# Kernel optimization log

Hardware: AMD Instinct MI355X
Metric: run time of the kernel (lower is better)

The kernel has to match this reference:

```python
import jax, jax.numpy as jnp
import numpy as np

B, C, H, W = 8, 256, 64, 64
CM = C // 4          # mask channels (theta/phi out) = 64
CI = C - CM          # img channels = 192
EPS = 1e-5


def setup_inputs() -> dict:
    key = jax.random.key(0)
    ks = jax.random.split(key, 12)
    return {
        "x": jax.random.normal(ks[0], (B, C, H, W), dtype=jnp.float32),
        "g_w": jax.random.normal(ks[1], (C, C), dtype=jnp.float32) * 0.05,
        "g_b": jax.random.normal(ks[2], (C,), dtype=jnp.float32) * 0.01,
        "theta_w": jax.random.normal(ks[3], (CM, CM), dtype=jnp.float32) * 0.1,
        "theta_b": jax.random.normal(ks[4], (CM,), dtype=jnp.float32) * 0.01,
        "phi_w": jax.random.normal(ks[5], (CM, CI), dtype=jnp.float32) * 0.06,
        "phi_b": jax.random.normal(ks[6], (CM,), dtype=jnp.float32) * 0.01,
        "W_w": jax.random.normal(ks[7], (C, C), dtype=jnp.float32) * 0.05,
        "W_b": jax.random.normal(ks[8], (C,), dtype=jnp.float32) * 0.01,
        "bn_gamma": jax.random.normal(ks[9], (C,), dtype=jnp.float32) * 0.1 + 1.0,
        "bn_beta": jax.random.normal(ks[10], (C,), dtype=jnp.float32) * 0.01,
        "bn_mean": jax.random.normal(ks[11], (C,), dtype=jnp.float32) * 0.1,
        "bn_var": jnp.ones((C,), dtype=jnp.float32),
    }


def _conv1x1(t, w, b):
    # [B,Cin,H,W] x [Cout,Cin] -> [B,Cout,H,W]
    return jnp.einsum('bchw,oc->bohw', t, w) + b[None, :, None, None]


def _maxpool2(t):
    b, c, h, w = t.shape
    return t.reshape(b, c, h // 2, 2, w // 2, 2).max(axis=(3, 5))


def reference(x, g_w, g_b, theta_w, theta_b, phi_w, phi_b, W_w, W_b,
              bn_gamma, bn_beta, bn_mean, bn_var):
    b, c, h, w = x.shape
    ci = c // 4
    mask_ch = x[:, :ci]          # [B, C/4, H, W]
    img_ch = x[:, ci:]           # [B, 3C/4, H, W]

    # g: conv1x1 then 2x2 maxpool -> [B, C, N'] -> [B, N', C]
    g_x = _maxpool2(_conv1x1(x, g_w, g_b)).reshape(b, c, -1).transpose(0, 2, 1)
    # theta: conv1x1 on mask -> [B, N, C/4]
    theta_x = _conv1x1(mask_ch, theta_w, theta_b).reshape(b, ci, -1).transpose(0, 2, 1)
    # phi: conv1x1 on img then pool -> [B, C/4, N']
    phi_x = _maxpool2(_conv1x1(img_ch, phi_w, phi_b)).reshape(b, ci, -1)

    f = jnp.einsum('bnc,bcm->bnm', theta_x, phi_x)     # [B, N, N']
    f_div_C = jax.nn.softmax(f, axis=-1)
    y = jnp.einsum('bnm,bmc->bnc', f_div_C, g_x)       # [B, N, C]
    y = y.transpose(0, 2, 1).reshape(b, c, h, w)

    W_y = _conv1x1(y, W_w, W_b)
    # BatchNorm (inference form with running stats)
    inv = jax.lax.rsqrt(bn_var + EPS)
    W_y = (W_y - bn_mean[None, :, None, None]) * (inv * bn_gamma)[None, :, None, None] \
          + bn_beta[None, :, None, None]
    return W_y + x
```

## Files before the change

### kernel.cpp

```cpp
#include <hip/hip_runtime.h>
#include <hip/hip_bf16.h>

typedef __hip_bfloat16 bf16;
typedef unsigned short ushort;
typedef unsigned int uint;
typedef __attribute__((ext_vector_type(8))) short short8;
typedef __attribute__((ext_vector_type(4))) float f32x4;

#define Bn 8
#define Cn 256
#define Nn 4096
#define Mn 1024
#define EPSf 1e-5f

__device__ __forceinline__ float b2f(const bf16 v){ return __bfloat162float(v); }
__device__ __forceinline__ ushort f2bu(float f){
  uint u = __float_as_uint(f);
  return (ushort)((u + 0x7FFFu + ((u >> 16) & 1u)) >> 16);
}

__global__ __launch_bounds__(256) void transpose_kernel(
    const float* __restrict__ x, bf16* __restrict__ xT)
{
  __shared__ float xs[64][65];
  const int t = threadIdx.x;
  const int p0 = blockIdx.x*64, c0 = blockIdx.y*64, b = blockIdx.z;
  #pragma unroll
  for (int i = 0; i < 16; ++i) {
    int idx = t + i*256; int cl = idx >> 6, pl = idx & 63;
    xs[cl][pl] = x[((long)(b*Cn) + c0 + cl)*Nn + p0 + pl];
  }
  __syncthreads();
  ushort* xTu = (ushort*)xT;
  #pragma unroll
  for (int i = 0; i < 8; ++i) {
    int idx = t + i*256; int pl = idx >> 5, cp = idx & 31;
    uint u = (uint)f2bu(xs[cp*2][pl]) | ((uint)f2bu(xs[cp*2+1][pl]) << 16);
    *(uint*)(xTu + ((long)(b*Nn) + p0 + pl)*Cn + c0 + cp*2) = u;
  }
}

__global__ __launch_bounds__(256) void wcomb_kernel(
    const float* __restrict__ tw, const float* __restrict__ tb,
    const float* __restrict__ pw, const float* __restrict__ pb,
    const float* __restrict__ gw, const float* __restrict__ gb,
    bf16* __restrict__ Wcomb, float* __restrict__ bcomb)
{
  const int r = blockIdx.x, c = threadIdx.x;
  float v;
  if (r < 64)        v = (c < 64)  ? tw[r*64 + c]            : 0.f;
  else if (r < 128)  v = (c >= 64) ? pw[(r-64)*192 + (c-64)] : 0.f;
  else               v = gw[(r-128)*256 + c];
  Wcomb[r*256 + c] = __float2bfloat16(v);
  if (c == 0)
    bcomb[r] = (r < 64) ? tb[r] : (r < 128) ? pb[r-64] : gb[r-128];
}

__global__ __launch_bounds__(256) void gemm384_kernel(
    const bf16* __restrict__ xT, const bf16* __restrict__ Wcomb,
    const float* __restrict__ bcomb, bf16* __restrict__ Q,
    bf16* __restrict__ K, bf16* __restrict__ Vt)
{
  __shared__ union {
    struct { ushort As[128*40]; ushort Bs[128*40]; } g;
    float Pb[2][128][33];
  } sm;
  const int t = threadIdx.x;
  const int px = blockIdx.x, o0 = blockIdx.y*128, b = blockIdx.z;
  const int p0 = px*128;
  const int lane = t & 63, w = t >> 6;
  const int ql = lane & 15, quad = lane >> 4;
  const int wm = (w & 1)*64, wn = (w >> 1)*64;
  const ushort* xTu = (const ushort*)xT;
  const ushort* Wu  = (const ushort*)Wcomb;

  f32x4 acc[4][4];
  #pragma unroll
  for (int i = 0; i < 4; ++i)
    #pragma unroll
    for (int j = 0; j < 4; ++j) acc[i][j] = (f32x4){0.f,0.f,0.f,0.f};

  for (int kc = 0; kc < 8; ++kc) {
    __syncthreads();
    #pragma unroll
    for (int i = 0; i < 2; ++i) {
      int idx = t + i*256; int r = idx >> 2, cq = idx & 3;
      *(uint4*)(sm.g.As + r*40 + cq*8) =
          *(const uint4*)(xTu + ((long)(b*Nn) + p0 + r)*Cn + kc*32 + cq*8);
      *(uint4*)(sm.g.Bs + r*40 + cq*8) =
          *(const uint4*)(Wu + (o0 + r)*Cn + kc*32 + cq*8);
    }
    __syncthreads();
    short8 aF[4], bF[4];
    #pragma unroll
    for (int mi = 0; mi < 4; ++mi)
      aF[mi] = *(const short8*)(sm.g.As + (wm + mi*16 + ql)*40 + quad*8);
    #pragma unroll
    for (int ni = 0; ni < 4; ++ni)
      bF[ni] = *(const short8*)(sm.g.Bs + (wn + ni*16 + ql)*40 + quad*8);
    #pragma unroll
    for (int mi = 0; mi < 4; ++mi)
      #pragma unroll
      for (int ni = 0; ni < 4; ++ni)
        acc[mi][ni] = __builtin_amdgcn_mfma_f32_16x16x32_bf16(aF[mi], bF[ni], acc[mi][ni], 0, 0, 0);
  }
  float bias[4];
  #pragma unroll
  for (int ni = 0; ni < 4; ++ni) bias[ni] = bcomb[o0 + wn + ni*16 + ql];

  if (o0 == 0 && wn == 0) {
    #pragma unroll
    for (int mi = 0; mi < 4; ++mi)
      #pragma unroll
      for (int ni = 0; ni < 4; ++ni)
        #pragma unroll
        for (int r = 0; r < 4; ++r) {
          int p = p0 + wm + mi*16 + quad*4 + r;
          Q[((long)(b*Nn) + p)*64 + ni*16 + ql] = __float2bfloat16(acc[mi][ni][r] + bias[ni]);
        }
  }
  __syncthreads();
  if (o0 != 0 || wn == 64) {
    int g = w & 1;
    #pragma unroll
    for (int mi = 0; mi < 4; ++mi)
      #pragma unroll
      for (int ni = 0; ni < 4; ++ni) {
        float a0 = acc[mi][ni][0] + bias[ni], a1 = acc[mi][ni][1] + bias[ni];
        float a2 = acc[mi][ni][2] + bias[ni], a3 = acc[mi][ni][3] + bias[ni];
        int o = wn + ni*16 + ql;
        int wp = mi*8 + quad*2;
        sm.Pb[g][o][wp]     = fmaxf(a0, a1);
        sm.Pb[g][o][wp + 1] = fmaxf(a2, a3);
      }
  }
  __syncthreads();
  if (o0 == 0) {
    int wp = t & 31, og = t >> 5;
    ushort kv[8];
    #pragma unroll
    for (int j = 0; j < 8; ++j) {
      int o = 64 + og*8 + j;
      kv[j] = f2bu(fmaxf(sm.Pb[0][o][wp], sm.Pb[1][o][wp]));
    }
    *(uint4*)((ushort*)K + ((long)(b*Mn) + px*32 + wp)*64 + og*8) = *(uint4*)kv;
  } else {
    int ol = t >> 1, wp0 = (t & 1)*16;
    ushort vv[16];
    #pragma unroll
    for (int j = 0; j < 16; ++j)
      vv[j] = f2bu(fmaxf(sm.Pb[0][ol][wp0 + j], sm.Pb[1][ol][wp0 + j]));
    ushort* dst = (ushort*)Vt + ((long)(b*Cn) + (o0 - 128) + ol)*Mn + px*32 + wp0;
    *(uint4*)dst       = *(uint4*)(vv);
    *(uint4*)(dst + 8) = *(uint4*)(vv + 8);
  }
}

__global__ __launch_bounds__(256) void attn_kernel(
    const bf16* __restrict__ Q, const bf16* __restrict__ K, const bf16* __restrict__ Vt,
    bf16* __restrict__ Y)
{
  __shared__ __align__(16) ushort Ks[64*68];
  __shared__ __align__(16) ushort Vs[256*68];
  __shared__ __align__(16) ushort Ps[64*68];
  __shared__ float l_sh[64];

  const int t = threadIdx.x;
  const int b = blockIdx.y, q0 = blockIdx.x*64;
  const int lane = t & 63, w = t >> 6;
  const int ql = lane & 15, quad = lane >> 4;
  const int rql = w*16;
  const int pvr = (w & 1)*32;
  const int pvc = (w >> 1)*128;
  const ushort* Qu = (const ushort*)Q;
  const ushort* Ku = (const ushort*)K;
  const ushort* Vu = (const ushort*)Vt;

  const long qrow = (long)(b*Nn) + q0 + rql + ql;
  short8 aQ0 = *(const short8*)(Qu + qrow*64 + quad*8);
  short8 aQ1 = *(const short8*)(Qu + qrow*64 + 32 + quad*8);

  float lrow[4];
  #pragma unroll
  for (int r = 0; r < 4; ++r) lrow[r] = 0.f;

  f32x4 acc[2][8];
  #pragma unroll
  for (int mi = 0; mi < 2; ++mi)
    #pragma unroll
    for (int ci = 0; ci < 8; ++ci) acc[mi][ci] = (f32x4){0.f,0.f,0.f,0.f};

  for (int mt = 0; mt < 16; ++mt) {
    const int m0 = mt*64;
    __syncthreads();
    {
      int ch = t & 7, rr = t >> 3;
      #pragma unroll
      for (int i = 0; i < 2; ++i) {
        int row = rr + 32*i;
        *(uint4*)(Ks + row*68 + ch*8) =
            *(const uint4*)(Ku + ((long)(b*Mn) + m0 + row)*64 + ch*8);
      }
      #pragma unroll
      for (int p = 0; p < 8; ++p) {
        int n = rr + 32*p;
        *(uint4*)(Vs + n*68 + ch*8) =
            *(const uint4*)(Vu + ((long)(b*Cn) + n)*Mn + m0 + ch*8);
      }
    }
    __syncthreads();
    #pragma unroll
    for (int ct = 0; ct < 4; ++ct) {
      short8 b0 = *(const short8*)(Ks + (ct*16 + ql)*68 + quad*8);
      short8 b1 = *(const short8*)(Ks + (ct*16 + ql)*68 + 32 + quad*8);
      f32x4 s = (f32x4){0.f,0.f,0.f,0.f};
      s = __builtin_amdgcn_mfma_f32_16x16x32_bf16(aQ0, b0, s, 0, 0, 0);
      s = __builtin_amdgcn_mfma_f32_16x16x32_bf16(aQ1, b1, s, 0, 0, 0);
      #pragma unroll
      for (int r = 0; r < 4; ++r) {
        float e = __expf(s[r]);
        lrow[r] += e;
        Ps[(rql + quad*4 + r)*68 + ct*16 + ql] = f2bu(e);
      }
    }
    __syncthreads();
    short8 aP0[2], aP1[2];
    #pragma unroll
    for (int mi = 0; mi < 2; ++mi) {
      aP0[mi] = *(const short8*)(Ps + (pvr + mi*16 + ql)*68 + quad*8);
      aP1[mi] = *(const short8*)(Ps + (pvr + mi*16 + ql)*68 + 32 + quad*8);
    }
    #pragma unroll
    for (int ci = 0; ci < 8; ++ci) {
      short8 b0 = *(const short8*)(Vs + (pvc + ci*16 + ql)*68 + quad*8);
      short8 b1 = *(const short8*)(Vs + (pvc + ci*16 + ql)*68 + 32 + quad*8);
      #pragma unroll
      for (int mi = 0; mi < 2; ++mi) {
        acc[mi][ci] = __builtin_amdgcn_mfma_f32_16x16x32_bf16(aP0[mi], b0, acc[mi][ci], 0, 0, 0);
        acc[mi][ci] = __builtin_amdgcn_mfma_f32_16x16x32_bf16(aP1[mi], b1, acc[mi][ci], 0, 0, 0);
      }
    }
  }
  #pragma unroll
  for (int r = 0; r < 4; ++r)
    #pragma unroll
    for (int off = 1; off < 16; off <<= 1)
      lrow[r] += __shfl_xor(lrow[r], off, 64);
  if (ql == 0) {
    #pragma unroll
    for (int r = 0; r < 4; ++r) l_sh[rql + quad*4 + r] = lrow[r];
  }
  __syncthreads();
  #pragma unroll
  for (int mi = 0; mi < 2; ++mi)
    #pragma unroll
    for (int r = 0; r < 4; ++r) {
      int row = pvr + mi*16 + quad*4 + r;
      float inv = 1.f / l_sh[row];
      #pragma unroll
      for (int ci = 0; ci < 8; ++ci)
        Y[((long)(b*Nn) + q0 + row)*256 + pvc + ci*16 + ql] = __float2bfloat16(acc[mi][ci][r]*inv);
    }
}

__global__ __launch_bounds__(256) void wconv_kernel(
    const bf16* __restrict__ Y, const float* __restrict__ Ww, const float* __restrict__ Wb,
    const float* __restrict__ gamma, const float* __restrict__ beta,
    const float* __restrict__ mean, const float* __restrict__ var,
    const float* __restrict__ x, float* __restrict__ out)
{
  __shared__ __align__(16) ushort As[128*40];
  __shared__ __align__(16) ushort Bs[128*40];
  __shared__ float ssc[128], ssh[128];
  const int t = threadIdx.x;
  const int n0 = blockIdx.x*128, o0 = blockIdx.y*128, b = blockIdx.z;
  const int lane = t & 63, w = t >> 6;
  const int ql = lane & 15, quad = lane >> 4;
  const int wm = (w & 1)*64, wn = (w >> 1)*64;
  const ushort* Yu = (const ushort*)Y;

  if (t < 128) {
    int o = o0 + t;
    float sc = gamma[o] * rsqrtf(var[o] + EPSf);
    ssc[t] = sc;
    ssh[t] = (Wb[o] - mean[o])*sc + beta[o];
  }

  f32x4 acc[4][4];
  #pragma unroll
  for (int i = 0; i < 4; ++i)
    #pragma unroll
    for (int j = 0; j < 4; ++j) acc[i][j] = (f32x4){0.f,0.f,0.f,0.f};

  for (int kc = 0; kc < 8; ++kc) {
    __syncthreads();
    #pragma unroll
    for (int i = 0; i < 4; ++i) {
      int idx = t + i*256; int r = idx >> 3, cq = idx & 7;
      float4 v = *(const float4*)(Ww + (o0 + r)*Cn + kc*32 + cq*4);
      uint lo = (uint)f2bu(v.x) | ((uint)f2bu(v.y) << 16);
      uint hi = (uint)f2bu(v.z) | ((uint)f2bu(v.w) << 16);
      *(uint2*)(As + r*40 + cq*4) = make_uint2(lo, hi);
    }
    #pragma unroll
    for (int i = 0; i < 2; ++i) {
      int idx = t + i*256; int r = idx >> 2, cq = idx & 3;
      *(uint4*)(Bs + r*40 + cq*8) =
          *(const uint4*)(Yu + ((long)(b*Nn) + n0 + r)*Cn + kc*32 + cq*8);
    }
    __syncthreads();
    short8 aF[4], bF[4];
    #pragma unroll
    for (int mi = 0; mi < 4; ++mi)
      aF[mi] = *(const short8*)(As + (wm + mi*16 + ql)*40 + quad*8);
    #pragma unroll
    for (int ni = 0; ni < 4; ++ni)
      bF[ni] = *(const short8*)(Bs + (wn + ni*16 + ql)*40 + quad*8);
    #pragma unroll
    for (int mi = 0; mi < 4; ++mi)
      #pragma unroll
      for (int ni = 0; ni < 4; ++ni)
        acc[mi][ni] = __builtin_amdgcn_mfma_f32_16x16x32_bf16(aF[mi], bF[ni], acc[mi][ni], 0, 0, 0);
  }
  #pragma unroll
  for (int mi = 0; mi < 4; ++mi)
    #pragma unroll
    for (int r = 0; r < 4; ++r) {
      int ol = wm + mi*16 + quad*4 + r;
      int o = o0 + ol;
      float sc = ssc[ol], sh = ssh[ol];
      #pragma unroll
      for (int ni = 0; ni < 4; ++ni) {
        int n = n0 + wn + ni*16 + ql;
        long gidx = ((long)(b*Cn + o))*Nn + n;
        out[gidx] = acc[mi][ni][r]*sc + sh + x[gidx];
      }
    }
}

extern "C" void kernel_launch(void* const* d_in, const int* in_sizes, int n_in,
                              void* d_out, int out_size, void* d_ws, size_t ws_size,
                              hipStream_t stream)
{
  const float* x       = (const float*)d_in[0];
  const float* g_w     = (const float*)d_in[1];
  const float* g_b     = (const float*)d_in[2];
  const float* theta_w = (const float*)d_in[3];
  const float* theta_b = (const float*)d_in[4];
  const float* phi_w   = (const float*)d_in[5];
  const float* phi_b   = (const float*)d_in[6];
  const float* W_w     = (const float*)d_in[7];
  const float* W_b     = (const float*)d_in[8];
  const float* bn_g    = (const float*)d_in[9];
  const float* bn_b    = (const float*)d_in[10];
  const float* bn_m    = (const float*)d_in[11];
  const float* bn_v    = (const float*)d_in[12];
  float* out = (float*)d_out;

  bf16* wsb = (bf16*)d_ws;
  bf16* xT    = wsb;
  bf16* Y     = wsb;
  bf16* Q     = wsb + 8388608;
  bf16* K     = wsb + 10485760;
  bf16* Vt    = wsb + 11010048;
  bf16* Wcomb = wsb + 13107200;
  float* bcomb = (float*)(wsb + 13205504);

  transpose_kernel<<<dim3(64, 4, Bn), 256, 0, stream>>>(x, xT);
  wcomb_kernel<<<dim3(384), 256, 0, stream>>>(theta_w, theta_b, phi_w, phi_b, g_w, g_b, Wcomb, bcomb);
  gemm384_kernel<<<dim3(32, 3, Bn), 256, 0, stream>>>(xT, Wcomb, bcomb, Q, K, Vt);
  attn_kernel<<<dim3(64, Bn), 256, 0, stream>>>(Q, K, Vt, Y);
  wconv_kernel<<<dim3(32, 2, Bn), 256, 0, stream>>>(Y, W_w, W_b, bn_g, bn_b, bn_m, bn_v, x, out);
}
```

Baseline: 186.2 us.

## Use 512 threads per attention block, splitting score keys and PV columns across 8 waves

The attention kernel goes from 4 to 8 wavefronts per block. Each wave computes scores for half of the 64 keys in a tile and accumulates a 32x64 slice of the PV output instead of 32x128. Row sums are combined from two partial buffers in shared memory. This halves per-thread accumulator registers and cooperative load work, raising parallelism and latency hiding for the 512-block grid, at the cost of more threads contending at each barrier.

New measurement: 185.1 us. Within noise of the previous version (-0.6%).

```diff
diff --git a/kernel.cpp b/kernel.cpp
--- a/kernel.cpp
+++ b/kernel.cpp
@@ -156,27 +156,28 @@
   }
 }
 
-__global__ __launch_bounds__(256) void attn_kernel(
+__global__ __launch_bounds__(512) void attn_kernel(
     const bf16* __restrict__ Q, const bf16* __restrict__ K, const bf16* __restrict__ Vt,
     bf16* __restrict__ Y)
 {
   __shared__ __align__(16) ushort Ks[64*68];
   __shared__ __align__(16) ushort Vs[256*68];
   __shared__ __align__(16) ushort Ps[64*68];
-  __shared__ float l_sh[64];
+  __shared__ float l_sh[2][64];
 
   const int t = threadIdx.x;
   const int b = blockIdx.y, q0 = blockIdx.x*64;
   const int lane = t & 63, w = t >> 6;
   const int ql = lane & 15, quad = lane >> 4;
-  const int rql = w*16;
-  const int pvr = (w & 1)*32;
-  const int pvc = (w >> 1)*128;
+  const int rt = w & 3;
+  const int kh = w >> 2;
+  const int rh = (w & 1)*32;
+  const int cq = (w >> 1)*64;
   const ushort* Qu = (const ushort*)Q;
   const ushort* Ku = (const ushort*)K;
   const ushort* Vu = (const ushort*)Vt;
 
-  const long qrow = (long)(b*Nn) + q0 + rql + ql;
+  const long qrow = (long)(b*Nn) + q0 + rt*16 + ql;
   short8 aQ0 = *(const short8*)(Qu + qrow*64 + quad*8);
   short8 aQ1 = *(const short8*)(Qu + qrow*64 + 32 + quad*8);
 
@@ -184,35 +185,32 @@
   #pragma unroll
   for (int r = 0; r < 4; ++r) lrow[r] = 0.f;
 
-  f32x4 acc[2][8];
+  f32x4 acc[2][4];
   #pragma unroll
   for (int mi = 0; mi < 2; ++mi)
     #pragma unroll
-    for (int ci = 0; ci < 8; ++ci) acc[mi][ci] = (f32x4){0.f,0.f,0.f,0.f};
+    for (int ci = 0; ci < 4; ++ci) acc[mi][ci] = (f32x4){0.f,0.f,0.f,0.f};
 
   for (int mt = 0; mt < 16; ++mt) {
     const int m0 = mt*64;
     __syncthreads();
     {
       int ch = t & 7, rr = t >> 3;
-      #pragma unroll
-      for (int i = 0; i < 2; ++i) {
-        int row = rr + 32*i;
-        *(uint4*)(Ks + row*68 + ch*8) =
-            *(const uint4*)(Ku + ((long)(b*Mn) + m0 + row)*64 + ch*8);
-      }
-      #pragma unroll
-      for (int p = 0; p < 8; ++p) {
-        int n = rr + 32*p;
+      *(uint4*)(Ks + rr*68 + ch*8) =
+          *(const uint4*)(Ku + ((long)(b*Mn) + m0 + rr)*64 + ch*8);
+      #pragma unroll
+      for (int p = 0; p < 4; ++p) {
+        int n = rr + 64*p;
         *(uint4*)(Vs + n*68 + ch*8) =
             *(const uint4*)(Vu + ((long)(b*Cn) + n)*Mn + m0 + ch*8);
       }
     }
     __syncthreads();
     #pragma unroll
-    for (int ct = 0; ct < 4; ++ct) {
-      short8 b0 = *(const short8*)(Ks + (ct*16 + ql)*68 + quad*8);
-      short8 b1 = *(const short8*)(Ks + (ct*16 + ql)*68 + 32 + quad*8);
+    for (int ct = 0; ct < 2; ++ct) {
+      int kb = kh*32 + ct*16;
+      short8 b0 = *(const short8*)(Ks + (kb + ql)*68 + quad*8);
+      short8 b1 = *(const short8*)(Ks + (kb + ql)*68 + 32 + quad*8);
       f32x4 s = (f32x4){0.f,0.f,0.f,0.f};
       s = __builtin_amdgcn_mfma_f32_16x16x32_bf16(aQ0, b0, s, 0, 0, 0);
       s = __builtin_amdgcn_mfma_f32_16x16x32_bf16(aQ1, b1, s, 0, 0, 0);
@@ -220,20 +218,20 @@
       for (int r = 0; r < 4; ++r) {
         float e = __expf(s[r]);
         lrow[r] += e;
-        Ps[(rql + quad*4 + r)*68 + ct*16 + ql] = f2bu(e);
+        Ps[(rt*16 + quad*4 + r)*68 + kb + ql] = f2bu(e);
       }
     }
     __syncthreads();
     short8 aP0[2], aP1[2];
     #pragma unroll
     for (int mi = 0; mi < 2; ++mi) {
-      aP0[mi] = *(const short8*)(Ps + (pvr + mi*16 + ql)*68 + quad*8);
-      aP1[mi] = *(const short8*)(Ps + (pvr + mi*16 + ql)*68 + 32 + quad*8);
-    }
-    #pragma unroll
-    for (int ci = 0; ci < 8; ++ci) {
-      short8 b0 = *(const short8*)(Vs + (pvc + ci*16 + ql)*68 + quad*8);
-      short8 b1 = *(const short8*)(Vs + (pvc + ci*16 + ql)*68 + 32 + quad*8);
+      aP0[mi] = *(const short8*)(Ps + (rh + mi*16 + ql)*68 + quad*8);
+      aP1[mi] = *(const short8*)(Ps + (rh + mi*16 + ql)*68 + 32 + quad*8);
+    }
+    #pragma unroll
+    for (int ci = 0; ci < 4; ++ci) {
+      short8 b0 = *(const short8*)(Vs + (cq + ci*16 + ql)*68 + quad*8);
+      short8 b1 = *(const short8*)(Vs + (cq + ci*16 + ql)*68 + 32 + quad*8);
       #pragma unroll
       for (int mi = 0; mi < 2; ++mi) {
         acc[mi][ci] = __builtin_amdgcn_mfma_f32_16x16x32_bf16(aP0[mi], b0, acc[mi][ci], 0, 0, 0);
@@ -248,18 +246,18 @@
       lrow[r] += __shfl_xor(lrow[r], off, 64);
   if (ql == 0) {
     #pragma unroll
-    for (int r = 0; r < 4; ++r) l_sh[rql + quad*4 + r] = lrow[r];
+    for (int r = 0; r < 4; ++r) l_sh[kh][rt*16 + quad*4 + r] = lrow[r];
   }
   __syncthreads();
   #pragma unroll
   for (int mi = 0; mi < 2; ++mi)
     #pragma unroll
     for (int r = 0; r < 4; ++r) {
-      int row = pvr + mi*16 + quad*4 + r;
-      float inv = 1.f / l_sh[row];
-      #pragma unroll
-      for (int ci = 0; ci < 8; ++ci)
-        Y[((long)(b*Nn) + q0 + row)*256 + pvc + ci*16 + ql] = __float2bfloat16(acc[mi][ci][r]*inv);
+      int row = rh + mi*16 + quad*4 + r;
+      float inv = 1.f / (l_sh[0][row] + l_sh[1][row]);
+      #pragma unroll
+      for (int ci = 0; ci < 4; ++ci)
+        Y[((long)(b*Nn) + q0 + row)*256 + cq + ci*16 + ql] = __float2bfloat16(acc[mi][ci][r]*inv);
     }
 }
 
@@ -369,6 +367,6 @@
   transpose_kernel<<<dim3(64, 4, Bn), 256, 0, stream>>>(x, xT);
   wcomb_kernel<<<dim3(384), 256, 0, stream>>>(theta_w, theta_b, phi_w, phi_b, g_w, g_b, Wcomb, bcomb);
   gemm384_kernel<<<dim3(32, 3, Bn), 256, 0, stream>>>(xT, Wcomb, bcomb, Q, K, Vt);
-  attn_kernel<<<dim3(64, Bn), 256, 0, stream>>>(Q, K, Vt, Y);
+  attn_kernel<<<dim3(64, Bn), 512, 0, stream>>>(Q, K, Vt, Y);
   wconv_kernel<<<dim3(32, 2, Bn), 256, 0, stream>>>(Y, W_w, W_b, bn_g, bn_b, bn_m, bn_v, x, out);
 }
```
